# Performance work log

Hardware: AMD Instinct MI355X
Metric: run time of the kernel (lower is better)

## Reference

```python
import jax, jax.numpy as jnp
import numpy as np

ETA = 0.1      # self.eta
BETA = 0.05    # self.beta
MU = 0.05      # self.mu
MINI = 1e-6    # mini_val
SEEDS_PER_TOPIC = 10


def setup_inputs() -> dict:
    key = jax.random.key(0)
    k1, k2, k3, k4 = jax.random.split(key, 4)
    B, V, K = 64, 10000, 64
    # sparse-ish bag-of-words counts in {0,1,2}
    batch_BOW = jax.random.randint(k1, (B, V), 0, 3).astype(jnp.float32)
    # disjoint seed words: SEEDS_PER_TOPIC seed words per topic
    seeds = jnp.zeros((V, K), jnp.float32)
    rows = jnp.arange(SEEDS_PER_TOPIC * K)
    cols = jnp.repeat(jnp.arange(K), SEEDS_PER_TOPIC)
    seeds = seeds.at[rows, cols].set(1.0)
    exp_m = jax.random.uniform(k2, (B, K), jnp.float32) * 10.0     # E[m_dk] for docs in batch
    exp_s = jax.random.uniform(k3, (V, K), jnp.float32) * 5.0 * seeds  # E[s_wk], nonzero only at seed entries
    exp_n = jax.random.uniform(k4, (V, K), jnp.float32) * 5.0      # E[n_wk]
    pi = jnp.full((K,), 0.7, jnp.float32)
    return {"batch_BOW": batch_BOW, "seeds": seeds, "exp_m": exp_m,
            "exp_s": exp_s, "exp_n": exp_n, "pi": pi}


def reference(batch_BOW, seeds, exp_m, exp_s, exp_n, pi):
    # Vectorized SCVB0_guided over the whole minibatch (no per-doc Python loop).
    V, K = seeds.shape
    S = seeds.sum(0)                      # [K] number of seed words per topic
    beta_sum = BETA * V                   # self.beta_sum[guided_m]
    mu_sum = MU * S                       # [K]
    exp_s_sum = exp_s.sum(0)              # [K]
    exp_n_sum = exp_n.sum(0)              # [K]

    mask = (batch_BOW > 0).astype(batch_BOW.dtype)[:, :, None]   # [B,V,1] BOW_nonzero gather
    theta = exp_m[:, None, :] + ETA                               # [B,1,K]
    phi_s = (MU + exp_s) / (mu_sum + exp_s_sum)                   # [V,K]
    phi_n = (BETA + exp_n) / (beta_sum + exp_n_sum)               # [V,K]

    g_ss = mask * seeds[None] * theta * phi_s[None] * pi          # [B,V,K]
    g_sr = mask * seeds[None] * theta * phi_n[None] * (1.0 - pi)
    g_rr = mask * (1.0 - seeds[None]) * theta * phi_n[None]

    s_sum = g_ss.sum(-1, keepdims=True) + g_sr.sum(-1, keepdims=True)
    r_sum = g_rr.sum(-1, keepdims=True)
    g_ss = g_ss / (s_sum + MINI)
    g_sr = g_sr / (s_sum + MINI)
    g_rr = g_rr / (r_sum + MINI)

    # seed word <=> word is seed of at least one topic; else use g_rr only
    is_seed = (seeds.sum(1) > 0)[None, :, None]                   # [1,V,1]
    gamma = jnp.where(is_seed, pi * g_ss + (1.0 - pi) * (g_sr + g_rr), g_rr)

    counts = batch_BOW[:, :, None]                                # [B,V,1]
    temp_exp_m_batch = (gamma * counts).sum(1)                    # [B,K]
    temp_exp_n = ((g_sr + g_rr) * counts).sum(0)                  # [V,K] scatter-accumulate
    temp_exp_s = (g_ss * counts).sum(0)                           # [V,K]
    gamma_sr_sum = g_sr.sum((0, 1))                               # [K]
    exp_q_z = (gamma * jnp.log(gamma + MINI)).sum()               # scalar entropy term
    return temp_exp_m_batch, temp_exp_n, temp_exp_s, gamma_sr_sum, exp_q_z
```

## Files before the change

### kernel.cpp

```cpp
#include <hip/hip_runtime.h>
#include <hip/hip_bf16.h>

#define ETA_C  0.1f
#define BETA_C 0.05f
#define MU_C   0.05f
#define MINI_C 1e-6f

typedef __attribute__((ext_vector_type(8))) short short8;
typedef __attribute__((ext_vector_type(4))) float f32x4;

template<int CTRL, int ROWMASK>
__device__ __forceinline__ float dpp_add(float x) {
  int v = __builtin_amdgcn_update_dpp(0, __float_as_int(x), CTRL, ROWMASK, 0xf, true);
  return x + __int_as_float(v);
}

__device__ __forceinline__ float wave_sum(float x) {
  x = dpp_add<0xB1,  0xF>(x);
  x = dpp_add<0x4E,  0xF>(x);
  x = dpp_add<0x141, 0xF>(x);
  x = dpp_add<0x140, 0xF>(x);
  x = dpp_add<0x142, 0xA>(x);
  x = dpp_add<0x143, 0xC>(x);
  return __int_as_float(__builtin_amdgcn_readlane(__float_as_int(x), 63));
}

__device__ __forceinline__ float rl(float x, int k) {
  return __int_as_float(__builtin_amdgcn_readlane(__float_as_int(x), k));
}

__device__ __forceinline__ short bf16r(float x) {
  unsigned u = __float_as_uint(x);
  u += 0x7fffu + ((u >> 16) & 1u);
  return (short)(u >> 16);
}

__device__ __forceinline__ float bf2f(short s) {
  return __uint_as_float(((unsigned)(unsigned short)s) << 16);
}

__global__ __launch_bounds__(256) void sums_kernel(
    const float* __restrict__ seeds, const float* __restrict__ es,
    const float* __restrict__ en, float* __restrict__ part,
    float* __restrict__ out, int V, int rows_per_block, int gsr_off) {
  __shared__ float sh[192];
  int t = threadIdx.x, bx = blockIdx.x;
  if (bx < 16) out[(bx << 8) + t] = 0.f;
  else if (bx == 16 && t < 65) out[gsr_off + t] = 0.f;
  if (t < 192) sh[t] = 0.f;
  __syncthreads();
  int k = t & 63, w = t >> 6;
  int v0 = bx * rows_per_block;
  int v1 = min(v0 + rows_per_block, V);
  float s0 = 0.f, s1 = 0.f, s2 = 0.f;
  for (int v = v0 + w; v < v1; v += 4) {
    int idx = (v << 6) + k;
    s0 += seeds[idx]; s1 += es[idx]; s2 += en[idx];
  }
  atomicAdd(&sh[k], s0);
  atomicAdd(&sh[64 + k], s1);
  atomicAdd(&sh[128 + k], s2);
  __syncthreads();
  if (t < 192) part[bx * 192 + t] = sh[t];
}

__global__ __launch_bounds__(1024, 4) void main_kernel(
    const float* __restrict__ bow,
    const float* __restrict__ seeds,
    const float* __restrict__ exp_m,
    const float* __restrict__ exp_s,
    const float* __restrict__ exp_n,
    const float* __restrict__ pi,
    const float* __restrict__ part,
    float* __restrict__ out,
    int V, int gsr_off, int NB) {
  __shared__ short THbf[4096];
  __shared__ short THTbf[4096];
  __shared__ short TLbf[4096];
  __shared__ short ARRT[1024];
  __shared__ short ASVT[1024];
  __shared__ short ARLT[1024];
  __shared__ short WSRT[2048];
  __shared__ short PKA[2048];
  __shared__ short CIRT[1024];
  __shared__ float RSL[64 * 17];
  __shared__ float SSL[64 * 17];
  __shared__ float L0a[64 * 17];
  __shared__ float L0b[64 * 17];
  __shared__ float sums_sh[192];
  float* NNL = RSL;
  float* red_gsr = SSL;
  float* redq = L0a;

  int t = threadIdx.x;
#pragma unroll
  for (int i = 0; i < 4; i++) {
    int idx = t + (i << 10);
    int b = idx >> 6, k = idx & 63;
    float th = exp_m[idx] + ETA_C;
    float lth = __logf(th);
    THbf[idx] = bf16r(th);
    THTbf[(k << 6) + b] = bf16r(th);
    TLbf[idx] = bf16r(th * lth);
  }
  if (t < 192) sums_sh[t] = 0.f;
  __syncthreads();
  {
    int grp = t >> 8;
    int col = t & 255;
    if (col < 192) {
      float s = 0.f;
#pragma unroll 16
      for (int i = 0; i < 64; i++) s += part[((grp << 6) + i) * 192 + col];
      atomicAdd(&sums_sh[col], s);
    }
  }
  __syncthreads();

  int lane = t & 63, w = t >> 6;
  int q = lane >> 4, c = lane & 15;
  float acc_g_tot = 0.f, acc_q_tot = 0.f;
  f32x4 accP = {0.f, 0.f, 0.f, 0.f};

  for (int tile = blockIdx.x; tile < NB; tile += gridDim.x) {
    int v = (tile << 4) + w;
    bool active = (v < V);

    float pik = 0.f, omp = 0.f, a_ss = 0.f, a_sr = 0.f, a_rr = 0.f;
    float bowpre = 0.f;
    bool seedRow = false;
    if (active) {
      int rbase = (v << 6) + lane;
      float seed = seeds[rbase];
      float es = exp_s[rbase];
      float en = exp_n[rbase];
      pik = pi[lane];
      float inv_ds = __builtin_amdgcn_rcpf(MU_C * sums_sh[lane] + sums_sh[64 + lane]);
      float inv_dn = __builtin_amdgcn_rcpf(BETA_C * (float)V + sums_sh[128 + lane]);
      float phi_s = (MU_C + es) * inv_ds;
      float phi_n = (BETA_C + en) * inv_dn;
      omp = 1.0f - pik;
      a_ss = seed * phi_s * pik;
      a_sr = seed * phi_n * omp;
      a_rr = (1.0f - seed) * phi_n;
      seedRow = (__ballot(seed > 0.f) != 0ull);
      float wsv = fmaf(pik, a_ss, omp * a_sr);
      float wrv = seedRow ? omp * a_rr : a_rr;
      float arrl = (a_rr > 0.f) ? a_rr * __logf(a_rr) : 0.f;
      ARRT[(w << 6) + lane] = bf16r(a_rr);
      ASVT[(w << 6) + lane] = bf16r(a_ss + a_sr);
      ARLT[(w << 6) + lane] = bf16r(arrl);
      WSRT[(lane << 5) + w] = bf16r(wsv);
      WSRT[(lane << 5) + 16 + w] = bf16r(wrv);
      bowpre = bow[lane * V + v];
    } else {
      ARRT[(w << 6) + lane] = 0;
      ASVT[(w << 6) + lane] = 0;
      ARLT[(w << 6) + lane] = 0;
      WSRT[(lane << 5) + w] = 0;
      WSRT[(lane << 5) + 16 + w] = 0;
    }
    __syncthreads();

    {
      int job = w >> 2, mt = w & 3;
      const short* Amat = (job == 3) ? TLbf : THbf;
      const short* Bmat = (job == 0) ? ARRT : (job == 1) ? ASVT
                         : (job == 2) ? ARLT : ARRT;
      float* Cd = (job == 0) ? RSL : (job == 1) ? SSL : (job == 2) ? L0a : L0b;
      f32x4 acc = {0.f, 0.f, 0.f, 0.f};
      int arow = (mt << 4) + c;
#pragma unroll
      for (int s = 0; s < 2; s++) {
        short8 af = *(const short8*)&Amat[(arow << 6) + (s << 5) + (q << 3)];
        short8 bf = *(const short8*)&Bmat[(c << 6) + (s << 5) + (q << 3)];
        acc = __builtin_amdgcn_mfma_f32_16x16x32_bf16(af, bf, acc, 0, 0, 0);
      }
#pragma unroll
      for (int r = 0; r < 4; r++)
        Cd[((mt << 4) + (q << 2) + r) * 17 + c] = acc[r];
    }
    __syncthreads();

    float acc_s = 0.f, acc_g = 0.f, acc_qk = 0.f, acc_qb = 0.f;
    if (active) {
      float rsv = RSL[lane * 17 + w];
      float ssv = SSL[lane * 17 + w];
      float ivx = __builtin_amdgcn_rcpf(ssv + MINI_C);
      float ivy = __builtin_amdgcn_rcpf(rsv + MINI_C);
      float cis = bowpre * ivx;
      float cirr = bowpre * ivy;
      PKA[(lane << 5) + w] = bf16r(cis);
      PKA[(lane << 5) + 16 + w] = bf16r(cirr);
      CIRT[(w << 6) + lane] = bf16r(cirr);
      if (!seedRow) {
        float Lb = L0a[lane * 17 + w] + L0b[lane * 17 + w];
        float q0 = (bowpre > 0.f) ? ivy : 0.f;
        float q1 = q0 * __logf(ivy);
        acc_qb = fmaf(q0, Lb, q1 * rsv);
        out[4096 + V * 64 + (v << 6) + lane] = 0.f;
      } else {
        float acc_n = 0.f;
        unsigned long long m = __ballot(bowpre > 0.f);
        while (m) {
          int b = __builtin_amdgcn_readfirstlane(__builtin_ctzll(m));
          m &= (m - 1);
          float cb = rl(bowpre, b);
          float is = rl(ivx, b), ir = rl(ivy, b);
          float th = bf2f(THbf[(b << 6) + lane]);
          float gss = th * a_ss * is;
          float gsr = th * a_sr * is;
          float grr = th * a_rr * ir;
          float gnr = gsr + grr;
          float gamma = fmaf(pik, gss, omp * gnr);
          acc_n = fmaf(gnr, cb, acc_n);
          acc_s = fmaf(gss, cb, acc_s);
          acc_g += gsr;
          acc_qk = fmaf(gamma, __logf(gamma + MINI_C), acc_qk);
        }
        out[4096 + (v << 6) + lane] = acc_n;
        out[4096 + V * 64 + (v << 6) + lane] = acc_s;
      }
    } else {
      PKA[(lane << 5) + w] = 0;
      PKA[(lane << 5) + 16 + w] = 0;
      CIRT[(w << 6) + lane] = 0;
    }
    acc_g_tot += acc_g;
    acc_q_tot += acc_qk + acc_qb;
    __syncthreads();

    {
      int tm = w >> 2, tn = w & 3;
      short8 af = *(const short8*)&PKA[(((tm << 4) + c) << 5) + (q << 3)];
      short8 bf = *(const short8*)&WSRT[(((tn << 4) + c) << 5) + (q << 3)];
      accP = __builtin_amdgcn_mfma_f32_16x16x32_bf16(af, bf, accP, 0, 0, 0);
      if (w >= 12) {
        int mt = w - 12;
        f32x4 an = {0.f, 0.f, 0.f, 0.f};
#pragma unroll
        for (int s = 0; s < 2; s++) {
          short8 a2 = *(const short8*)&THTbf[(((mt << 4) + c) << 6) + (s << 5) + (q << 3)];
          short8 b2 = *(const short8*)&CIRT[(c << 6) + (s << 5) + (q << 3)];
          an = __builtin_amdgcn_mfma_f32_16x16x32_bf16(a2, b2, an, 0, 0, 0);
        }
#pragma unroll
        for (int r = 0; r < 4; r++)
          NNL[((mt << 4) + (q << 2) + r) * 17 + c] = an[r];
      }
    }
    __syncthreads();

    if (active && !seedRow)
      out[4096 + (v << 6) + lane] = a_rr * NNL[lane * 17 + w];
  }

  {
    int tm = w >> 2, tn = w & 3;
#pragma unroll
    for (int r = 0; r < 4; r++) {
      int brow = (tm << 4) + (q << 2) + r;
      int kcol = (tn << 4) + c;
      float val = accP[r] * bf2f(THbf[(brow << 6) + kcol]);
      atomicAdd(&out[(brow << 6) + kcol], val);
    }
  }
  __syncthreads();
  red_gsr[t] = acc_g_tot;
  float qzw = wave_sum(acc_q_tot);
  if (lane == 0) redq[w] = qzw;
  __syncthreads();

  if (w == 0) {
    float g = 0.f;
#pragma unroll
    for (int j = 0; j < 16; j++) g += red_gsr[(j << 6) + lane];
    if (g != 0.f) atomicAdd(&out[gsr_off + lane], g);
    if (t == 0) {
      float qs = 0.f;
#pragma unroll
      for (int j = 0; j < 16; j++) qs += redq[j];
      atomicAdd(&out[gsr_off + 64], qs);
    }
  }
}

extern "C" void kernel_launch(void* const* d_in, const int* in_sizes, int n_in,
                              void* d_out, int out_size, void* d_ws,
                              size_t ws_size, hipStream_t stream) {
  (void)n_in; (void)out_size; (void)ws_size;
  const float* bow   = (const float*)d_in[0];
  const float* seeds = (const float*)d_in[1];
  const float* exp_m = (const float*)d_in[2];
  const float* exp_s = (const float*)d_in[3];
  const float* exp_n = (const float*)d_in[4];
  const float* pi    = (const float*)d_in[5];
  int K = in_sizes[5];
  int V = in_sizes[1] / K;
  float* out = (float*)d_out;
  float* part = (float*)d_ws;

  int NB = (V + 15) / 16;
  int NP = NB < 512 ? NB : 512;
  int gsr_off = 4096 + 2 * V * 64;
  int rpb = (V + 255) / 256;

  sums_kernel<<<256, 256, 0, stream>>>(seeds, exp_s, exp_n, part, out, V, rpb,
                                       gsr_off);
  main_kernel<<<NP, 1024, 0, stream>>>(bow, seeds, exp_m, exp_s, exp_n, pi,
                                       part, out, V, gsr_off, NB);
}
```

Before: 106.8 us.

## Prefetch all tile inputs upfront and replace global atomics with staged reduction

```diff
diff --git a/kernel.cpp b/kernel.cpp
--- a/kernel.cpp
+++ b/kernel.cpp
@@ -45,8 +45,7 @@
     float* __restrict__ out, int V, int rows_per_block, int gsr_off) {
   __shared__ float sh[192];
   int t = threadIdx.x, bx = blockIdx.x;
-  if (bx < 16) out[(bx << 8) + t] = 0.f;
-  else if (bx == 16 && t < 65) out[gsr_off + t] = 0.f;
+  if (bx == 16 && t < 65) out[gsr_off + t] = 0.f;
   if (t < 192) sh[t] = 0.f;
   __syncthreads();
   int k = t & 63, w = t >> 6;
@@ -72,6 +71,8 @@
     const float* __restrict__ exp_n,
     const float* __restrict__ pi,
     const float* __restrict__ part,
+    float* __restrict__ stage,
+    float* __restrict__ qzst,
     float* __restrict__ out,
     int V, int gsr_off, int NB) {
   __shared__ short THbf[4096];
@@ -93,6 +94,31 @@
   float* redq = L0a;
 
   int t = threadIdx.x;
+  int lane = t & 63, w = t >> 6;
+
+  int gd = (int)gridDim.x;
+  float sd[3], esv[3], env[3], bwv[3];
+  int nt = 0;
+#pragma unroll
+  for (int i = 0; i < 3; i++) {
+    int tile = (int)blockIdx.x + i * gd;
+    if (tile < NB) {
+      nt = i + 1;
+      int v = (tile << 4) + w;
+      if (v < V) {
+        int rbase = (v << 6) + lane;
+        sd[i]  = seeds[rbase];
+        esv[i] = exp_s[rbase];
+        env[i] = exp_n[rbase];
+        bwv[i] = bow[lane * V + v];
+      } else {
+        sd[i] = 0.f; esv[i] = 0.f; env[i] = 0.f; bwv[i] = 0.f;
+      }
+    }
+  }
+  float pik = pi[lane];
+  float omp = 1.0f - pik;
+
 #pragma unroll
   for (int i = 0; i < 4; i++) {
     int idx = t + (i << 10);
@@ -117,29 +143,28 @@
   }
   __syncthreads();
 
-  int lane = t & 63, w = t >> 6;
   int q = lane >> 4, c = lane & 15;
   float acc_g_tot = 0.f, acc_q_tot = 0.f;
   f32x4 accP = {0.f, 0.f, 0.f, 0.f};
 
-  for (int tile = blockIdx.x; tile < NB; tile += gridDim.x) {
+#pragma unroll
+  for (int it = 0; it < 3; it++) {
+    if (it >= nt) break;
+    int tile = (int)blockIdx.x + it * gd;
     int v = (tile << 4) + w;
     bool active = (v < V);
 
-    float pik = 0.f, omp = 0.f, a_ss = 0.f, a_sr = 0.f, a_rr = 0.f;
-    float bowpre = 0.f;
+    float a_ss = 0.f, a_sr = 0.f, a_rr = 0.f;
+    float bowpre = bwv[it];
     bool seedRow = false;
     if (active) {
-      int rbase = (v << 6) + lane;
-      float seed = seeds[rbase];
-      float es = exp_s[rbase];
-      float en = exp_n[rbase];
-      pik = pi[lane];
+      float seed = sd[it];
+      float es = esv[it];
+      float en = env[it];
       float inv_ds = __builtin_amdgcn_rcpf(MU_C * sums_sh[lane] + sums_sh[64 + lane]);
       float inv_dn = __builtin_amdgcn_rcpf(BETA_C * (float)V + sums_sh[128 + lane]);
       float phi_s = (MU_C + es) * inv_ds;
       float phi_n = (BETA_C + en) * inv_dn;
-      omp = 1.0f - pik;
       a_ss = seed * phi_s * pik;
       a_sr = seed * phi_n * omp;
       a_rr = (1.0f - seed) * phi_n;
@@ -152,7 +177,6 @@
       ARLT[(w << 6) + lane] = bf16r(arrl);
       WSRT[(lane << 5) + w] = bf16r(wsv);
       WSRT[(lane << 5) + 16 + w] = bf16r(wrv);
-      bowpre = bow[lane * V + v];
     } else {
       ARRT[(w << 6) + lane] = 0;
       ASVT[(w << 6) + lane] = 0;
@@ -256,13 +280,13 @@
   }
 
   {
+    float* so = stage + ((int)blockIdx.x << 12);
     int tm = w >> 2, tn = w & 3;
 #pragma unroll
     for (int r = 0; r < 4; r++) {
       int brow = (tm << 4) + (q << 2) + r;
       int kcol = (tn << 4) + c;
-      float val = accP[r] * bf2f(THbf[(brow << 6) + kcol]);
-      atomicAdd(&out[(brow << 6) + kcol], val);
+      so[(brow << 6) + kcol] = accP[r] * bf2f(THbf[(brow << 6) + kcol]);
     }
   }
   __syncthreads();
@@ -280,8 +304,41 @@
       float qs = 0.f;
 #pragma unroll
       for (int j = 0; j < 16; j++) qs += redq[j];
-      atomicAdd(&out[gsr_off + 64], qs);
-    }
+      qzst[blockIdx.x] = qs;
+    }
+  }
+}
+
+__global__ __launch_bounds__(256) void finalize_kernel(
+    const float* __restrict__ stage, const float* __restrict__ qzst,
+    float* __restrict__ out, int gsr_off, int NP) {
+  __shared__ float red[256];
+  int t = threadIdx.x, bx = blockIdx.x;
+  int col = t & 15, xg = t >> 4;
+  float s = 0.f;
+  int x0 = xg << 4;
+#pragma unroll
+  for (int j = 0; j < 16; j++) {
+    int x = x0 + j;
+    if (x < NP) s += stage[(x << 12) + (bx << 4) + col];
+  }
+  red[t] = s;
+  __syncthreads();
+  if (t < 16) {
+    float r = 0.f;
+#pragma unroll
+    for (int j = 0; j < 16; j++) r += red[(j << 4) + t];
+    out[(bx << 4) + t] = r;
+  }
+  if (bx == 0 && t < 64) {
+    float qv = 0.f;
+#pragma unroll
+    for (int j = 0; j < 4; j++) {
+      int x = t + (j << 6);
+      if (x < NP) qv += qzst[x];
+    }
+    qv = wave_sum(qv);
+    if (t == 0) out[gsr_off + 64] = qv;
   }
 }
 
@@ -298,15 +355,18 @@
   int K = in_sizes[5];
   int V = in_sizes[1] / K;
   float* out = (float*)d_out;
-  float* part = (float*)d_ws;
+  float* part  = (float*)d_ws;
+  float* stage = part + 256 * 192;
+  float* qzst  = stage + 256 * 4096;
 
   int NB = (V + 15) / 16;
-  int NP = NB < 512 ? NB : 512;
+  int NP = NB < 256 ? NB : 256;
   int gsr_off = 4096 + 2 * V * 64;
   int rpb = (V + 255) / 256;
 
   sums_kernel<<<256, 256, 0, stream>>>(seeds, exp_s, exp_n, part, out, V, rpb,
                                        gsr_off);
   main_kernel<<<NP, 1024, 0, stream>>>(bow, seeds, exp_m, exp_s, exp_n, pi,
-                                       part, out, V, gsr_off, NB);
-}
+                                       part, stage, qzst, out, V, gsr_off, NB);
+  finalize_kernel<<<256, 256, 0, stream>>>(stage, qzst, out, gsr_off, NP);
+}
```

Result: slower. 111.7 us (+4.6%).

## Prefetch per-tile inputs before sums reduction, transpose partials, halve grid

Applied to the files above, without the earlier changes.

```diff
diff --git a/kernel.cpp b/kernel.cpp
--- a/kernel.cpp
+++ b/kernel.cpp
@@ -61,7 +61,7 @@
   atomicAdd(&sh[64 + k], s1);
   atomicAdd(&sh[128 + k], s2);
   __syncthreads();
-  if (t < 192) part[bx * 192 + t] = sh[t];
+  if (t < 192) part[t * 256 + bx] = sh[t];
 }
 
 __global__ __launch_bounds__(1024, 4) void main_kernel(
@@ -93,6 +93,31 @@
   float* redq = L0a;
 
   int t = threadIdx.x;
+  int lane = t & 63, w = t >> 6;
+
+  int gd = (int)gridDim.x;
+  float sd[3], esv[3], env[3], bwv[3];
+  int nt = 0;
+#pragma unroll
+  for (int i = 0; i < 3; i++) {
+    int tile = (int)blockIdx.x + i * gd;
+    if (tile < NB) {
+      nt = i + 1;
+      int v = (tile << 4) + w;
+      if (v < V) {
+        int rbase = (v << 6) + lane;
+        sd[i]  = seeds[rbase];
+        esv[i] = exp_s[rbase];
+        env[i] = exp_n[rbase];
+        bwv[i] = bow[lane * V + v];
+      } else {
+        sd[i] = 0.f; esv[i] = 0.f; env[i] = 0.f; bwv[i] = 0.f;
+      }
+    }
+  }
+  float pik = pi[lane];
+  float omp = 1.0f - pik;
+
 #pragma unroll
   for (int i = 0; i < 4; i++) {
     int idx = t + (i << 10);
@@ -105,41 +130,42 @@
   }
   if (t < 192) sums_sh[t] = 0.f;
   __syncthreads();
-  {
-    int grp = t >> 8;
-    int col = t & 255;
-    if (col < 192) {
-      float s = 0.f;
-#pragma unroll 16
-      for (int i = 0; i < 64; i++) s += part[((grp << 6) + i) * 192 + col];
-      atomicAdd(&sums_sh[col], s);
-    }
-  }
-  __syncthreads();
-
-  int lane = t & 63, w = t >> 6;
+  if (t < 768) {
+    int col = t % 192;
+    int seg = t / 192;
+    const f32x4* p = (const f32x4*)&part[col * 256 + (seg << 6)];
+    float s = 0.f;
+#pragma unroll
+    for (int j = 0; j < 16; j++) {
+      f32x4 v4 = p[j];
+      s += (v4[0] + v4[1]) + (v4[2] + v4[3]);
+    }
+    atomicAdd(&sums_sh[col], s);
+  }
+  __syncthreads();
+
   int q = lane >> 4, c = lane & 15;
   float acc_g_tot = 0.f, acc_q_tot = 0.f;
   f32x4 accP = {0.f, 0.f, 0.f, 0.f};
 
-  for (int tile = blockIdx.x; tile < NB; tile += gridDim.x) {
+#pragma unroll
+  for (int it = 0; it < 3; it++) {
+    if (it >= nt) break;
+    int tile = (int)blockIdx.x + it * gd;
     int v = (tile << 4) + w;
     bool active = (v < V);
 
-    float pik = 0.f, omp = 0.f, a_ss = 0.f, a_sr = 0.f, a_rr = 0.f;
-    float bowpre = 0.f;
+    float a_ss = 0.f, a_sr = 0.f, a_rr = 0.f;
+    float bowpre = bwv[it];
     bool seedRow = false;
     if (active) {
-      int rbase = (v << 6) + lane;
-      float seed = seeds[rbase];
-      float es = exp_s[rbase];
-      float en = exp_n[rbase];
-      pik = pi[lane];
+      float seed = sd[it];
+      float es = esv[it];
+      float en = env[it];
       float inv_ds = __builtin_amdgcn_rcpf(MU_C * sums_sh[lane] + sums_sh[64 + lane]);
       float inv_dn = __builtin_amdgcn_rcpf(BETA_C * (float)V + sums_sh[128 + lane]);
       float phi_s = (MU_C + es) * inv_ds;
       float phi_n = (BETA_C + en) * inv_dn;
-      omp = 1.0f - pik;
       a_ss = seed * phi_s * pik;
       a_sr = seed * phi_n * omp;
       a_rr = (1.0f - seed) * phi_n;
@@ -152,7 +178,6 @@
       ARLT[(w << 6) + lane] = bf16r(arrl);
       WSRT[(lane << 5) + w] = bf16r(wsv);
       WSRT[(lane << 5) + 16 + w] = bf16r(wrv);
-      bowpre = bow[lane * V + v];
     } else {
       ARRT[(w << 6) + lane] = 0;
       ASVT[(w << 6) + lane] = 0;
@@ -301,7 +326,7 @@
   float* part = (float*)d_ws;
 
   int NB = (V + 15) / 16;
-  int NP = NB < 512 ? NB : 512;
+  int NP = NB < 256 ? NB : 256;
   int gsr_off = 4096 + 2 * V * 64;
   int rpb = (V + 255) / 256;
 
```

Result: no change. 105.2 us (-1.5%).
